# Optimization experiments

Measured on AMD Instinct MI355X. Metric: run time of the kernel, lower is better.

The kernel has to match this reference:

```python
import jax, jax.numpy as jnp
import numpy as np

EPS = 1e-12  # matches torch F.normalize default eps (clamp_min)
B, C, N = 32, 512, 4096
K_CLUSTERS, G_CLUSTERS = 64, 8
T_CLUSTERS = K_CLUSTERS + G_CLUSTERS  # 72
H_ATTN = T_CLUSTERS // 4  # 18


def _l2norm(v, axis):
    return v / jnp.maximum(jnp.linalg.norm(v, axis=axis, keepdims=True), EPS)


def setup_inputs() -> dict:
    key = jax.random.key(0)
    ks = jax.random.split(key, 6)
    x = jax.random.normal(ks[0], (B, C, N), dtype=jnp.float32)
    centroids = jax.random.normal(ks[1], (T_CLUSTERS, C), dtype=jnp.float32) * 0.01
    # 1x1 Conv2d(C -> T) == dense [T, C] weight + bias
    conv_w = jax.random.normal(ks[2], (T_CLUSTERS, C), dtype=jnp.float32) / np.sqrt(C).astype(np.float32)
    conv_b = jnp.zeros((T_CLUSTERS,), dtype=jnp.float32)
    ghost_weights = jnp.ones((G_CLUSTERS,), dtype=jnp.float32) * 0.1
    w1 = jax.random.normal(ks[3], (H_ATTN, T_CLUSTERS), dtype=jnp.float32) / np.sqrt(T_CLUSTERS).astype(np.float32)
    b1 = jnp.zeros((H_ATTN,), dtype=jnp.float32)
    w2 = jax.random.normal(ks[4], (T_CLUSTERS, H_ATTN), dtype=jnp.float32) / np.sqrt(H_ATTN).astype(np.float32)
    b2 = jnp.zeros((T_CLUSTERS,), dtype=jnp.float32)
    return {"x": x, "centroids": centroids, "conv_w": conv_w, "conv_b": conv_b,
            "ghost_weights": ghost_weights, "w1": w1, "b1": b1, "w2": w2, "b2": b2}


def reference(x, centroids, conv_w, conv_b, ghost_weights, w1, b1, w2, b2):
    # x: [B, C, N] -> L2 normalize over channel dim
    xn = _l2norm(x, axis=1)
    # 1x1 conv -> soft assignment logits [B, T, N], softmax over clusters
    logits = jnp.einsum('kc,bcn->bkn', conv_w, xn) + conv_b[None, :, None]
    assign = jax.nn.softmax(logits, axis=1)
    # residual aggregation, algebraically fused:
    # vlad[b,k,c] = sum_n a[b,k,n]*x[b,c,n] - centroid[k,c]*sum_n a[b,k,n]
    agg = jnp.einsum('bkn,bcn->bkc', assign, xn)
    mass = assign.sum(axis=-1)  # [B, T]
    vlad = agg - centroids[None, :, :] * mass[:, :, None]
    # ghost cluster down-weighting
    gw = jax.nn.softmax(ghost_weights)
    vlad = vlad.at[:, K_CLUSTERS:, :].multiply(gw[None, :, None])
    # attention over clusters: mean over C -> MLP -> softmax over clusters
    scores = vlad.mean(axis=-1)  # [B, T]
    h = jax.nn.relu(scores @ w1.T + b1)
    attn = jax.nn.softmax(h @ w2.T + b2, axis=1)
    vlad = vlad * attn[:, :, None]
    # intra-cluster L2 norm, drop ghosts, flatten, global L2 norm
    vlad = _l2norm(vlad, axis=2)
    vlad = vlad[:, :K_CLUSTERS, :].reshape(vlad.shape[0], -1)
    return _l2norm(vlad, axis=1)
```

## Files before the change

kernel.cpp:

```cpp
#include <hip/hip_runtime.h>
#include <hip/hip_bf16.h>

#define B_ 32
#define C_ 512
#define N_ 4096
#define T_ 72
#define K_ 64
#define KP 80
#define EPSF 1e-12f

typedef unsigned short u16;
typedef unsigned int u32;
typedef __attribute__((ext_vector_type(8))) short bf16x8;
typedef __attribute__((ext_vector_type(4))) float f32x4;

__device__ __forceinline__ u16 f2bf(float v) {
    __hip_bfloat16 h = __float2bfloat16(v);
    return *reinterpret_cast<u16*>(&h);
}

__global__ __launch_bounds__(256) void k_prep(
    const float* __restrict__ conv_w, const float* __restrict__ conv_b,
    u16* __restrict__ Wp, float* __restrict__ bp)
{
    const int idx = blockIdx.x * 256 + threadIdx.x;
    if (idx < KP * C_) {
        const int k = idx >> 9, c = idx & (C_ - 1);
        Wp[idx] = f2bf(k < T_ ? conv_w[k * C_ + c] : 0.f);
    } else if (idx < KP * C_ + KP) {
        const int j = idx - KP * C_;
        bp[j] = (j < T_) ? conv_b[j] : -1e30f;
    }
}

#define ANW 256
__global__ __launch_bounds__(256, 2) void k_assign(
    const float* __restrict__ x, const u16* __restrict__ Wp,
    const float* __restrict__ bp, u16* __restrict__ assignp,
    float* __restrict__ mass)
{
    __shared__ u16   xs[ANW * 32];
    __shared__ float red[4][ANW];
    __shared__ float inv_sh[ANW];

    const int t = threadIdx.x;
    const int b = blockIdx.y;
    const int n0 = blockIdx.x * ANW;
    const int lane = t & 63, w = t >> 6;
    const int q = lane >> 4, nl = lane & 15;

    const float* xb = x + (size_t)b * C_ * N_ + n0 + 4 * lane;

    f32x4 acc[4][5];
    #pragma unroll
    for (int nt = 0; nt < 4; ++nt)
        #pragma unroll
        for (int mt = 0; mt < 5; ++mt) acc[nt][mt] = (f32x4)0.f;
    float ss[4] = {0.f, 0.f, 0.f, 0.f};

    float4 v[8];
    bf16x8 af[5];
    #pragma unroll
    for (int i = 0; i < 8; ++i)
        v[i] = *(const float4*)(xb + (size_t)(w * 8 + i) * N_);
    #pragma unroll
    for (int mt = 0; mt < 5; ++mt)
        af[mt] = *(const bf16x8*)(Wp + (size_t)(mt * 16 + nl) * C_ + q * 8);

#define VJ(i) (j == 0 ? v[i].x : j == 1 ? v[i].y : j == 2 ? v[i].z : v[i].w)

    #pragma unroll 1
    for (int ch = 0; ch < 16; ++ch) {
        #pragma unroll
        for (int j = 0; j < 4; ++j) {
            const float f0 = VJ(0), f1 = VJ(1), f2 = VJ(2), f3 = VJ(3);
            const float f4 = VJ(4), f5 = VJ(5), f6 = VJ(6), f7 = VJ(7);
            ss[j] = fmaf(f0, f0, ss[j]); ss[j] = fmaf(f1, f1, ss[j]);
            ss[j] = fmaf(f2, f2, ss[j]); ss[j] = fmaf(f3, f3, ss[j]);
            ss[j] = fmaf(f4, f4, ss[j]); ss[j] = fmaf(f5, f5, ss[j]);
            ss[j] = fmaf(f6, f6, ss[j]); ss[j] = fmaf(f7, f7, ss[j]);
            uint4 pk;
            pk.x = (u32)f2bf(f0) | ((u32)f2bf(f1) << 16);
            pk.y = (u32)f2bf(f2) | ((u32)f2bf(f3) << 16);
            pk.z = (u32)f2bf(f4) | ((u32)f2bf(f5) << 16);
            pk.w = (u32)f2bf(f6) | ((u32)f2bf(f7) << 16);
            const int n = 4 * lane + j;
            const int slot = (w + ((lane >> 1) & 3)) & 3;
            *(uint4*)&xs[n * 32 + slot * 8] = pk;
        }
        __syncthreads();
        if (ch < 15) {
            #pragma unroll
            for (int i = 0; i < 8; ++i)
                v[i] = *(const float4*)(xb + (size_t)((ch + 1) * 32 + w * 8 + i) * N_);
        }
        __builtin_amdgcn_sched_barrier(0);
        #pragma unroll
        for (int nt = 0; nt < 4; ++nt) {
            const int n = (4 * w + nt) * 16 + nl;
            const int slot = (q + ((n >> 3) & 3)) & 3;
            const bf16x8 bfr = *(const bf16x8*)&xs[n * 32 + slot * 8];
            #pragma unroll
            for (int mt = 0; mt < 5; ++mt)
                acc[nt][mt] = __builtin_amdgcn_mfma_f32_16x16x32_bf16(af[mt], bfr, acc[nt][mt], 0, 0, 0);
        }
        if (ch < 15) {
            #pragma unroll
            for (int mt = 0; mt < 5; ++mt)
                af[mt] = *(const bf16x8*)(Wp + (size_t)(mt * 16 + nl) * C_ + (ch + 1) * 32 + q * 8);
        }
        __syncthreads();
    }
#undef VJ

    *(float4*)&red[w][4 * lane] = make_float4(ss[0], ss[1], ss[2], ss[3]);
    __syncthreads();
    {
        const float s = red[0][t] + red[1][t] + red[2][t] + red[3][t];
        inv_sh[t] = 1.0f / fmaxf(sqrtf(s), EPSF);
    }
    __syncthreads();

    float bpv[5][4];
    #pragma unroll
    for (int mt = 0; mt < 5; ++mt)
        #pragma unroll
        for (int r = 0; r < 4; ++r) bpv[mt][r] = bp[mt * 16 + q * 4 + r];

    #pragma unroll
    for (int nt = 0; nt < 4; ++nt) {
        const int n_loc = (4 * w + nt) * 16 + nl;
        const float invn = inv_sh[n_loc];
        const int nglob = n0 + n_loc;

        float lg[5][4];
        #pragma unroll
        for (int mt = 0; mt < 5; ++mt)
            #pragma unroll
            for (int r = 0; r < 4; ++r)
                lg[mt][r] = acc[nt][mt][r] * invn + bpv[mt][r];

        float mx = -1e30f;
        #pragma unroll
        for (int mt = 0; mt < 5; ++mt)
            #pragma unroll
            for (int r = 0; r < 4; ++r) mx = fmaxf(mx, lg[mt][r]);
        mx = fmaxf(mx, __shfl_xor(mx, 16, 64));
        mx = fmaxf(mx, __shfl_xor(mx, 32, 64));

        float s = 0.f;
        #pragma unroll
        for (int mt = 0; mt < 5; ++mt)
            #pragma unroll
            for (int r = 0; r < 4; ++r) {
                lg[mt][r] = __expf(lg[mt][r] - mx);
                s += lg[mt][r];
            }
        s += __shfl_xor(s, 16, 64);
        s += __shfl_xor(s, 32, 64);
        const float rs = 1.0f / s;

        #pragma unroll
        for (int mt = 0; mt < 4; ++mt)
            #pragma unroll
            for (int r = 0; r < 4; ++r) {
                const float a = lg[mt][r] * rs;
                float msum = a;
                msum += __shfl_xor(msum, 1, 64);
                msum += __shfl_xor(msum, 2, 64);
                msum += __shfl_xor(msum, 4, 64);
                msum += __shfl_xor(msum, 8, 64);
                const int k = mt * 16 + q * 4 + r;
                if (nl == 0) atomicAdd(&mass[b * K_ + k], msum);
                assignp[((size_t)b * K_ + k) * N_ + nglob] = f2bf(a * invn);
            }
    }
}

#define AGW 1024
#define AGS 256
#define AGP 264
__global__ __launch_bounds__(256) void k_agg(
    const float* __restrict__ x, const u16* __restrict__ assignp,
    float* __restrict__ out)
{
    __shared__ u16 Bt[K_][AGP];

    const int t = threadIdx.x, b = blockIdx.z;
    const int nc0 = blockIdx.y * AGW;
    const int c0 = blockIdx.x * 64;
    const int lane = t & 63, w = t >> 6;
    const int q = lane >> 4, nl = lane & 15;

    f32x4 acc[4];
    #pragma unroll
    for (int mt = 0; mt < 4; ++mt) acc[mt] = (f32x4)0.f;

    const u16*   ab = assignp + (size_t)b * K_ * N_ + (size_t)nl * N_ + q * 8;
    const float* xb = x + ((size_t)b * C_ + c0) * N_;

    #pragma unroll 1
    for (int p = 0; p < AGW / AGS; ++p) {
        const int n0 = nc0 + p * AGS;
        #pragma unroll
        for (int i = 0; i < 16; ++i) {
            const int cr = 16 * w + i;
            const float4 vv = *(const float4*)(xb + (size_t)cr * N_ + n0 + 4 * lane);
            uint2 pk;
            pk.x = (u32)f2bf(vv.x) | ((u32)f2bf(vv.y) << 16);
            pk.y = (u32)f2bf(vv.z) | ((u32)f2bf(vv.w) << 16);
            *(uint2*)&Bt[cr][4 * lane] = pk;
        }
        __syncthreads();
        #pragma unroll
        for (int ks = 0; ks < 8; ++ks) {
            const bf16x8 bfr = *(const bf16x8*)&Bt[16 * w + nl][ks * 32 + q * 8];
            #pragma unroll
            for (int mt = 0; mt < 4; ++mt) {
                const bf16x8 afv = *(const bf16x8*)(ab + (size_t)(mt * 16) * N_ + n0 + ks * 32);
                acc[mt] = __builtin_amdgcn_mfma_f32_16x16x32_bf16(afv, bfr, acc[mt], 0, 0, 0);
            }
        }
        __syncthreads();
    }

    float* ob = out + (size_t)b * K_ * C_;
    const int c = c0 + 16 * w + nl;
    #pragma unroll
    for (int mt = 0; mt < 4; ++mt)
        #pragma unroll
        for (int r = 0; r < 4; ++r)
            atomicAdd(&ob[(size_t)(mt * 16 + q * 4 + r) * C_ + c], acc[mt][r]);
}

__device__ __forceinline__ float block_reduce_sum_256(float v) {
    #pragma unroll
    for (int o = 32; o > 0; o >>= 1) v += __shfl_down(v, o, 64);
    __shared__ float wsh[4];
    const int lane = threadIdx.x & 63, wid = threadIdx.x >> 6;
    if (lane == 0) wsh[wid] = v;
    __syncthreads();
    float r = 0.f;
    if (threadIdx.x == 0) r = wsh[0] + wsh[1] + wsh[2] + wsh[3];
    return r;
}

__global__ __launch_bounds__(256) void k_rnorm(
    const float* __restrict__ agg, const float* __restrict__ centroids,
    const float* __restrict__ mass, float* __restrict__ rnorm,
    float* __restrict__ gsum)
{
    const int k = blockIdx.x, b = blockIdx.y;
    const float mk = mass[b * K_ + k];
    const float* p  = agg + ((size_t)b * K_ + k) * C_;
    const float* cb = centroids + k * C_;
    float s = 0.f;
    #pragma unroll 2
    for (int i = threadIdx.x; i < C_; i += 256) {
        const float v = fmaf(-cb[i], mk, p[i]);
        s = fmaf(v, v, s);
    }
    const float ss = block_reduce_sum_256(s);
    if (threadIdx.x == 0) {
        const float rn = fmaxf(sqrtf(ss), EPSF);
        rnorm[b * K_ + k] = rn;
        atomicAdd(gsum + b, ss / (rn * rn));
    }
}

__global__ __launch_bounds__(256) void k_final(
    float* __restrict__ out, const float* __restrict__ centroids,
    const float* __restrict__ mass, const float* __restrict__ rnorm,
    const float* __restrict__ gsum)
{
    const size_t i4 = ((size_t)blockIdx.x * 256 + threadIdx.x) * 4;
    const int b = (int)(i4 >> 15);
    const int k = (int)((i4 >> 9) & 63);
    const int c = (int)(i4 & 511);
    const float gn = fmaxf(sqrtf(gsum[b]), EPSF);
    const float sc = 1.0f / (rnorm[b * K_ + k] * gn);
    const float mk = mass[b * K_ + k];
    float4 v  = *(const float4*)(out + i4);
    const float4 cv = *(const float4*)(centroids + k * C_ + c);
    v.x = fmaf(-cv.x, mk, v.x) * sc;
    v.y = fmaf(-cv.y, mk, v.y) * sc;
    v.z = fmaf(-cv.z, mk, v.z) * sc;
    v.w = fmaf(-cv.w, mk, v.w) * sc;
    *(float4*)(out + i4) = v;
}

extern "C" void kernel_launch(void* const* d_in, const int* in_sizes, int n_in,
                              void* d_out, int out_size, void* d_ws, size_t ws_size,
                              hipStream_t stream) {
    const float* x         = (const float*)d_in[0];
    const float* centroids = (const float*)d_in[1];
    const float* conv_w    = (const float*)d_in[2];
    const float* conv_b    = (const float*)d_in[3];

    float* out = (float*)d_out;
    char*  ws  = (char*)d_ws;

    u16*   assignp = (u16*)ws;
    u16*   Wp      = (u16*)(ws + 16777216);
    float* bpad    = (float*)(ws + 16777216 + 81920);
    float* mass    = (float*)(ws + 16777216 + 81920 + 320);
    float* rnorm   = mass + B_ * K_;
    float* gsum    = rnorm + B_ * K_;

    hipMemsetAsync(mass, 0, B_ * K_ * sizeof(float), stream);
    hipMemsetAsync(gsum, 0, B_ * sizeof(float), stream);
    hipMemsetAsync(out, 0, (size_t)out_size * sizeof(float), stream);

    k_prep<<<dim3((KP * C_ + KP + 255) / 256), 256, 0, stream>>>(conv_w, conv_b, Wp, bpad);
    k_assign<<<dim3(N_ / ANW, B_), 256, 0, stream>>>(x, Wp, bpad, assignp, mass);
    k_agg<<<dim3(C_ / 64, N_ / AGW, B_), 256, 0, stream>>>(x, assignp, out);
    k_rnorm<<<dim3(K_, B_), 256, 0, stream>>>(out, centroids, mass, rnorm, gsum);
    k_final<<<(out_size / 4 + 255) / 256, 256, 0, stream>>>(out, centroids, mass, rnorm, gsum);
}
```

Measured before the change: 509.8 us.

## Stage assignment tiles in LDS and prefetch next chunk into registers in k_agg

The aggregation kernel now also stages the bf16 assignment tile in shared memory instead of having each wave read it straight from global memory. Both the x and assignment tiles for the next chunk are prefetched into registers while the MFMAs run on the current chunk. The chunk size is halved to keep LDS and register use bounded. This is meant to hide global-load latency and cut redundant global reads of the assignment matrix, at the cost of more registers and more barrier iterations.

Measured after the change: 517.0 us. About the same (+1.4%).

```diff
diff --git a/kernel.cpp b/kernel.cpp
--- a/kernel.cpp
+++ b/kernel.cpp
@@ -178,12 +178,13 @@
 }
 
 #define AGW 1024
-#define AGS 256
-#define AGP 264
+#define AGS 128
+#define AGP 136
 __global__ __launch_bounds__(256) void k_agg(
     const float* __restrict__ x, const u16* __restrict__ assignp,
     float* __restrict__ out)
 {
+    __shared__ u16 At[K_][AGP];
     __shared__ u16 Bt[K_][AGP];
 
     const int t = threadIdx.x, b = blockIdx.z;
@@ -192,32 +193,55 @@
     const int lane = t & 63, w = t >> 6;
     const int q = lane >> 4, nl = lane & 15;
 
+    const int as = lane & 15, ar = lane >> 4;
+    const int bs = lane & 31, br = lane >> 5;
+
     f32x4 acc[4];
     #pragma unroll
     for (int mt = 0; mt < 4; ++mt) acc[mt] = (f32x4)0.f;
 
-    const u16*   ab = assignp + (size_t)b * K_ * N_ + (size_t)nl * N_ + q * 8;
+    const u16*   ab = assignp + (size_t)b * K_ * N_;
     const float* xb = x + ((size_t)b * C_ + c0) * N_;
 
+    uint4  ra[4];
+    float4 rb[8];
+    #pragma unroll
+    for (int i = 0; i < 4; ++i)
+        ra[i] = *(const uint4*)(ab + (size_t)(16 * w + 4 * i + ar) * N_ + nc0 + as * 8);
+    #pragma unroll
+    for (int i = 0; i < 8; ++i)
+        rb[i] = *(const float4*)(xb + (size_t)(16 * w + 2 * i + br) * N_ + nc0 + bs * 4);
+
     #pragma unroll 1
-    for (int p = 0; p < AGW / AGS; ++p) {
-        const int n0 = nc0 + p * AGS;
-        #pragma unroll
-        for (int i = 0; i < 16; ++i) {
-            const int cr = 16 * w + i;
-            const float4 vv = *(const float4*)(xb + (size_t)cr * N_ + n0 + 4 * lane);
+    for (int ph = 0; ph < AGW / AGS; ++ph) {
+        #pragma unroll
+        for (int i = 0; i < 4; ++i)
+            *(uint4*)&At[16 * w + 4 * i + ar][as * 8] = ra[i];
+        #pragma unroll
+        for (int i = 0; i < 8; ++i) {
+            const float4 vv = rb[i];
             uint2 pk;
             pk.x = (u32)f2bf(vv.x) | ((u32)f2bf(vv.y) << 16);
             pk.y = (u32)f2bf(vv.z) | ((u32)f2bf(vv.w) << 16);
-            *(uint2*)&Bt[cr][4 * lane] = pk;
+            *(uint2*)&Bt[16 * w + 2 * i + br][bs * 4] = pk;
         }
         __syncthreads();
-        #pragma unroll
-        for (int ks = 0; ks < 8; ++ks) {
+        if (ph < AGW / AGS - 1) {
+            const int n1 = nc0 + (ph + 1) * AGS;
+            #pragma unroll
+            for (int i = 0; i < 4; ++i)
+                ra[i] = *(const uint4*)(ab + (size_t)(16 * w + 4 * i + ar) * N_ + n1 + as * 8);
+            #pragma unroll
+            for (int i = 0; i < 8; ++i)
+                rb[i] = *(const float4*)(xb + (size_t)(16 * w + 2 * i + br) * N_ + n1 + bs * 4);
+        }
+        __builtin_amdgcn_sched_barrier(0);
+        #pragma unroll
+        for (int ks = 0; ks < 4; ++ks) {
             const bf16x8 bfr = *(const bf16x8*)&Bt[16 * w + nl][ks * 32 + q * 8];
             #pragma unroll
             for (int mt = 0; mt < 4; ++mt) {
-                const bf16x8 afv = *(const bf16x8*)(ab + (size_t)(mt * 16) * N_ + n0 + ks * 32);
+                const bf16x8 afv = *(const bf16x8*)&At[mt * 16 + nl][ks * 32 + q * 8];
                 acc[mt] = __builtin_amdgcn_mfma_f32_16x16x32_bf16(afv, bfr, acc[mt], 0, 0, 0);
             }
         }
```
